# Kernel optimization log

Measured on AMD Instinct MI355X. Metric: run time of the kernel, lower is better.

Reference implementation:

```python
import jax, jax.numpy as jnp
import numpy as np

P, K, L = 2048, 10, 3        # pairs, paths-per-pair (cap 10), max path length
E, H = 256, 512              # kg_embed_dim, node_dim
N_ENT, N_REL = 10000, 200
N_HEADS = 4


def setup_inputs() -> dict:
    key = jax.random.key(0)
    ks = jax.random.split(key, 20)
    s = 0.05  # weight scale for numerical stability
    return {
        'rel_idx': jax.random.randint(ks[0], (P, K, L), 0, N_REL, dtype=jnp.int32),
        'ent_idx': jax.random.randint(ks[1], (P, K, L), 0, N_ENT, dtype=jnp.int32),
        'path_lens': jax.random.randint(ks[2], (P, K), 0, L + 1, dtype=jnp.int32),
        'rel_table': jax.random.normal(ks[3], (N_REL, E), jnp.float32),
        'ent_table': jax.random.normal(ks[4], (N_ENT, E), jnp.float32),
        'kg_proj_w': jax.random.normal(ks[5], (H, E), jnp.float32) * s,
        'kg_proj_b': jax.random.normal(ks[6], (H,), jnp.float32) * s,
        'w_ih': jax.random.normal(ks[7], (4 * H, 2 * H), jnp.float32) * s,
        'w_hh': jax.random.normal(ks[8], (4 * H, H), jnp.float32) * s,
        'b_ih': jax.random.normal(ks[9], (4 * H,), jnp.float32) * s,
        'b_hh': jax.random.normal(ks[10], (4 * H,), jnp.float32) * s,
        'attn_in_w': jax.random.normal(ks[11], (3 * H, H), jnp.float32) * s,
        'attn_in_b': jax.random.normal(ks[12], (3 * H,), jnp.float32) * s,
        'attn_out_w': jax.random.normal(ks[13], (H, H), jnp.float32) * s,
        'attn_out_b': jax.random.normal(ks[14], (H,), jnp.float32) * s,
        'path_proj_w': jax.random.normal(ks[15], (H, H), jnp.float32) * s,
        'path_proj_b': jax.random.normal(ks[16], (H,), jnp.float32) * s,
    }


def _forward(rel_idx, ent_idx, path_lens, rel_table, ent_table, kg_proj_w, kg_proj_b,
             w_ih, w_hh, b_ih, b_hh, attn_in_w, attn_in_b, attn_out_w, attn_out_b,
             path_proj_w, path_proj_b):
    # --- encode_path, batched over all P*K paths ---
    rel_e = rel_table[rel_idx]                      # [P,K,L,E]
    ent_e = ent_table[ent_idx]                      # [P,K,L,E]
    rel_p = rel_e @ kg_proj_w.T + kg_proj_b         # [P,K,L,H]
    ent_p = ent_e @ kg_proj_w.T + kg_proj_b
    x = jnp.concatenate([rel_p, ent_p], axis=-1)    # [P,K,L,2H]
    Npk = P * K
    xs = x.reshape(Npk, L, 2 * H).transpose(1, 0, 2)  # [L,N,2H]

    h0 = jnp.zeros((Npk, H), x.dtype)
    c0 = jnp.zeros((Npk, H), x.dtype)

    def lstm_step(carry, x_t):
        h, c = carry
        g = x_t @ w_ih.T + b_ih + h @ w_hh.T + b_hh   # [N,4H], torch gate order i,f,g,o
        i, f, gg, o = jnp.split(g, 4, axis=-1)
        c = jax.nn.sigmoid(f) * c + jax.nn.sigmoid(i) * jnp.tanh(gg)
        h = jax.nn.sigmoid(o) * jnp.tanh(c)
        return (h, c), h

    _, hs = jax.lax.scan(lstm_step, (h0, c0), xs)     # [L,N,H]
    hs = hs.transpose(1, 0, 2)                        # [N,L,H]
    lens = path_lens.reshape(Npk)                     # [N]
    last = jnp.clip(lens - 1, 0, L - 1)
    h_last = jnp.take_along_axis(hs, last[:, None, None], axis=1)[:, 0]  # [N,H]
    path_emb = jnp.where(lens[:, None] > 0, h_last, 0.0).reshape(P, K, H)

    # --- per-pair multi-head self-attention over K path embeddings ---
    wq, wk, wv = jnp.split(attn_in_w, 3, axis=0)
    bq, bk, bv = jnp.split(attn_in_b, 3, axis=0)
    Dh = H // N_HEADS
    q = (path_emb @ wq.T + bq).reshape(P, K, N_HEADS, Dh)
    k = (path_emb @ wk.T + bk).reshape(P, K, N_HEADS, Dh)
    v = (path_emb @ wv.T + bv).reshape(P, K, N_HEADS, Dh)
    scores = jnp.einsum('pqhd,pkhd->phqk', q, k) / jnp.sqrt(jnp.array(Dh, x.dtype))
    attn = jax.nn.softmax(scores, axis=-1)
    ctx = jnp.einsum('phqk,pkhd->pqhd', attn, v).reshape(P, K, H)
    attn_out = ctx @ attn_out_w.T + attn_out_b        # [P,K,H]
    agg = attn_out.mean(axis=1)                       # [P,H]  (aggregated.mean(dim=1))
    return agg @ path_proj_w.T + path_proj_b          # [P,H]


def reference(rel_idx, ent_idx, path_lens, rel_table, ent_table, kg_proj_w, kg_proj_b,
              w_ih, w_hh, b_ih, b_hh, attn_in_w, attn_in_b, attn_out_w, attn_out_b,
              path_proj_w, path_proj_b):
    return _forward(rel_idx, ent_idx, path_lens, rel_table, ent_table, kg_proj_w,
                    kg_proj_b, w_ih, w_hh, b_ih, b_hh, attn_in_w, attn_in_b,
                    attn_out_w, attn_out_b, path_proj_w, path_proj_b)
```

## Files before the change

### kernel.cpp

```cpp
#include <hip/hip_runtime.h>
#include <cstdint>
#include <cstddef>

#define PP 2048
#define KK 10
#define HH 512
#define NPK (PP*KK)
#define ENT_PAD 10112
#define REL_PAD 256
#define HALF_PAIRS 1024
#define HALF_ROWS (HALF_PAIRS*KK)

using f32x4  = __attribute__((ext_vector_type(4))) float;
using short8 = __attribute__((ext_vector_type(8))) short;

__device__ __forceinline__ float fexp2(float x) {
#if __has_builtin(__builtin_amdgcn_exp2f)
    return __builtin_amdgcn_exp2f(x);
#else
    return __exp2f(x);
#endif
}
__device__ __forceinline__ float frcp(float x) {
#if __has_builtin(__builtin_amdgcn_rcpf)
    return __builtin_amdgcn_rcpf(x);
#else
    return 1.0f / x;
#endif
}
#define LOG2E  1.4426950408889634f
#define LOG2E2 2.8853900817779268f
__device__ __forceinline__ float sigf(float x) {
    return frcp(1.0f + fexp2(-LOG2E * x));
}
__device__ __forceinline__ float tanhf_f(float x) {
    float xc = fminf(fmaxf(x, -9.0f), 9.0f);
    float e = fexp2(LOG2E2 * xc);
    return (e - 1.0f) * frcp(e + 1.0f);
}

__device__ __forceinline__ ushort f2bf(float x) {
    union { float f; uint32_t u; } v; v.f = x;
    uint32_t r = v.u + 0x7FFF + ((v.u >> 16) & 1);
    return (ushort)(r >> 16);
}
__device__ __forceinline__ float bf2f(ushort u) {
    union { uint32_t u; float f; } v; v.u = ((uint32_t)u) << 16;
    return v.f;
}

__global__ __launch_bounds__(256) void perm_bias2(int* __restrict__ perm_p,
                                                  int* __restrict__ perm_q,
                                                  float* __restrict__ bihh_q,
                                                  const float* __restrict__ b_ih,
                                                  const float* __restrict__ b_hh) {
    int i = blockIdx.x * 256 + threadIdx.x;
    if (i < 2048) {
        int uh = i >> 6, g = (i >> 4) & 3, ul = i & 15;
        perm_p[i] = g * 512 + uh * 16 + ul;
        int u = i >> 2, gq = i & 3;
        int oldq = gq * 512 + u;
        perm_q[i] = oldq;
        bihh_q[i] = b_ih[oldq] + b_hh[oldq];
    }
}

__global__ __launch_bounds__(256) void transpose_k(const float* __restrict__ src,
                                                   float* __restrict__ dst, int R, int C) {
    __shared__ float t[32][33];
    int bx = blockIdx.x * 32, by = blockIdx.y * 32;
    int x = threadIdx.x & 31, y = threadIdx.x >> 5;
    for (int i = y; i < 32; i += 8) {
        int r = by + i, c = bx + x;
        if (r < R && c < C) t[i][x] = src[(size_t)r * C + c];
    }
    __syncthreads();
    for (int i = y; i < 32; i += 8) {
        int c = bx + i, r = by + x;
        if (r < R && c < C) dst[(size_t)c * R + r] = t[x][i];
    }
}

__global__ __launch_bounds__(256) void rowdot(const float* __restrict__ A, int lda,
                                              const float* __restrict__ vec, int Kd,
                                              const float* __restrict__ add1,
                                              float* __restrict__ out, int M) {
    int w = threadIdx.x >> 6, lane = threadIdx.x & 63;
    int row = blockIdx.x * 4 + w;
    if (row >= M) return;
    float acc = 0.f;
    for (int k = lane; k < Kd; k += 64) acc += A[(size_t)row * lda + k] * vec[k];
    for (int off = 32; off; off >>= 1) acc += __shfl_down(acc, off, 64);
    if (lane == 0) {
        float r = acc;
        if (add1) r += add1[row];
        out[row] = r;
    }
}

__global__ __launch_bounds__(256) void f2bf_split2d(const float* __restrict__ src,
                                                    int lda, int col0,
                                                    ushort* __restrict__ hi,
                                                    ushort* __restrict__ lo,
                                                    int nsrc_rows, int ncols, int ndst_rows,
                                                    const int* __restrict__ perm) {
    int i = blockIdx.x * 256 + threadIdx.x;
    int nc4 = ncols >> 2;
    if (i >= ndst_rows * nc4) return;
    int row = i / nc4, c4 = i % nc4;
    ushort4 h = make_ushort4(0, 0, 0, 0), l = make_ushort4(0, 0, 0, 0);
    if (row < nsrc_rows) {
        int sr = perm ? perm[row] : row;
        float4 v = *reinterpret_cast<const float4*>(src + (size_t)sr * lda + col0 + c4 * 4);
        h = make_ushort4(f2bf(v.x), f2bf(v.y), f2bf(v.z), f2bf(v.w));
        l = make_ushort4(f2bf(v.x - bf2f(h.x)), f2bf(v.y - bf2f(h.y)),
                         f2bf(v.z - bf2f(h.z)), f2bf(v.w - bf2f(h.w)));
    }
    reinterpret_cast<ushort4*>(hi)[i] = h;
    reinterpret_cast<ushort4*>(lo)[i] = l;
}

__global__ __launch_bounds__(256) void f2bf_k(const float* __restrict__ s,
                                              ushort* __restrict__ d, int n4) {
    int i = blockIdx.x * 256 + threadIdx.x;
    if (i < n4) {
        float4 v = reinterpret_cast<const float4*>(s)[i];
        reinterpret_cast<ushort4*>(d)[i] = make_ushort4(f2bf(v.x), f2bf(v.y), f2bf(v.z), f2bf(v.w));
    }
}

__global__ __launch_bounds__(256) void f2bf_perm_rows(const float* __restrict__ s,
                                                      ushort* __restrict__ d,
                                                      const int* __restrict__ perm,
                                                      int nrows, int ncols4) {
    int i = blockIdx.x * 256 + threadIdx.x;
    if (i >= nrows * ncols4) return;
    int row = i / ncols4, c4 = i % ncols4;
    int sr = perm[row];
    float4 v = reinterpret_cast<const float4*>(s + (size_t)sr * ncols4 * 4)[c4];
    reinterpret_cast<ushort4*>(d + (size_t)row * ncols4 * 4)[c4] =
        make_ushort4(f2bf(v.x), f2bf(v.y), f2bf(v.z), f2bf(v.w));
}

__global__ __launch_bounds__(256) void gemm_bf16(
    const ushort* __restrict__ A, const ushort* __restrict__ B,
    float* __restrict__ C, int M, int N, int K, int ldc,
    const float* __restrict__ bias)
{
    __shared__ ushort As[128 * 64];
    __shared__ ushort Bs[128 * 64];
    int tid = threadIdx.x;
    int lane = tid & 63;
    int w = tid >> 6;
    int wr = w >> 1, wc = w & 1;
    int col0 = blockIdx.x * 128, row0 = blockIdx.y * 128;

    f32x4 acc[4][4];
#pragma unroll
    for (int m = 0; m < 4; ++m)
#pragma unroll
        for (int n = 0; n < 4; ++n) acc[m][n] = {0.f, 0.f, 0.f, 0.f};

    int rA = lane & 15;
    int kq = lane >> 4;

    for (int kt = 0; kt < K; kt += 64) {
#pragma unroll
        for (int it = 0; it < 4; ++it) {
            int c = it * 256 + tid;
            int row = c >> 3, ch = c & 7;
            int cs = ch ^ (row & 7);
            uint4 va = *reinterpret_cast<const uint4*>(A + (size_t)(row0 + row) * K + kt + ch * 8);
            *reinterpret_cast<uint4*>(&As[(size_t)row * 64 + cs * 8]) = va;
            uint4 vb = *reinterpret_cast<const uint4*>(B + (size_t)(col0 + row) * K + kt + ch * 8);
            *reinterpret_cast<uint4*>(&Bs[(size_t)row * 64 + cs * 8]) = vb;
        }
        __syncthreads();
#pragma unroll
        for (int s = 0; s < 2; ++s) {
            int csw = (s * 4 + kq) ^ (rA & 7);
            short8 af[4], bfr[4];
#pragma unroll
            for (int m = 0; m < 4; ++m) {
                int rowA = wr * 64 + m * 16 + rA;
                af[m] = *reinterpret_cast<const short8*>(&As[(size_t)rowA * 64 + csw * 8]);
            }
#pragma unroll
            for (int n = 0; n < 4; ++n) {
                int rowB = wc * 64 + n * 16 + rA;
                bfr[n] = *reinterpret_cast<const short8*>(&Bs[(size_t)rowB * 64 + csw * 8]);
            }
#pragma unroll
            for (int m = 0; m < 4; ++m)
#pragma unroll
                for (int n = 0; n < 4; ++n)
                    acc[m][n] = __builtin_amdgcn_mfma_f32_16x16x32_bf16(af[m], bfr[n], acc[m][n], 0, 0, 0);
        }
        __syncthreads();
    }
#pragma unroll
    for (int n = 0; n < 4; ++n) {
        int gcol = col0 + wc * 64 + n * 16 + rA;
        float bv = bias ? bias[gcol] : 0.f;
#pragma unroll
        for (int m = 0; m < 4; ++m) {
            int grow0 = row0 + wr * 64 + m * 16 + kq * 4;
#pragma unroll
            for (int r = 0; r < 4; ++r)
                C[(size_t)(grow0 + r) * ldc + gcol] = acc[m][n][r] + bv;
        }
    }
}

__global__ __launch_bounds__(256) void gemm_bf16s(
    const ushort* __restrict__ Ah, const ushort* __restrict__ Al,
    const ushort* __restrict__ Bh, const ushort* __restrict__ Bl,
    float* __restrict__ C, ushort* __restrict__ Chi, ushort* __restrict__ Clo,
    int M, int N, int K, int ldc,
    const float* __restrict__ bias)
{
    __shared__ ushort Ash[128 * 64];
    __shared__ ushort Asl[128 * 64];
    __shared__ ushort Bsh[128 * 64];
    __shared__ ushort Bsl[128 * 64];
    int tid = threadIdx.x;
    int lane = tid & 63;
    int w = tid >> 6;
    int wr = w >> 1, wc = w & 1;
    int col0 = blockIdx.x * 128, row0 = blockIdx.y * 128;

    f32x4 acc[4][4];
#pragma unroll
    for (int m = 0; m < 4; ++m)
#pragma unroll
        for (int n = 0; n < 4; ++n) acc[m][n] = {0.f, 0.f, 0.f, 0.f};

    int rA = lane & 15;
    int kq = lane >> 4;

    for (int kt = 0; kt < K; kt += 64) {
#pragma unroll
        for (int it = 0; it < 4; ++it) {
            int c = it * 256 + tid;
            int row = c >> 3, ch = c & 7;
            int cs = ch ^ (row & 7);
            size_t ga = (size_t)(row0 + row) * K + kt + ch * 8;
            size_t gb = (size_t)(col0 + row) * K + kt + ch * 8;
            size_t la = (size_t)row * 64 + cs * 8;
            *reinterpret_cast<uint4*>(&Ash[la]) = *reinterpret_cast<const uint4*>(Ah + ga);
            *reinterpret_cast<uint4*>(&Asl[la]) = *reinterpret_cast<const uint4*>(Al + ga);
            *reinterpret_cast<uint4*>(&Bsh[la]) = *reinterpret_cast<const uint4*>(Bh + gb);
            *reinterpret_cast<uint4*>(&Bsl[la]) = *reinterpret_cast<const uint4*>(Bl + gb);
        }
        __syncthreads();
#pragma unroll
        for (int s = 0; s < 2; ++s) {
            int csw = (s * 4 + kq) ^ (rA & 7);
            short8 xh[4], yh[4], t4[4];
#pragma unroll
            for (int m = 0; m < 4; ++m) {
                int rowA = wr * 64 + m * 16 + rA;
                xh[m] = *reinterpret_cast<const short8*>(&Ash[(size_t)rowA * 64 + csw * 8]);
            }
#pragma unroll
            for (int n = 0; n < 4; ++n) {
                int rowB = wc * 64 + n * 16 + rA;
                yh[n] = *reinterpret_cast<const short8*>(&Bsh[(size_t)rowB * 64 + csw * 8]);
            }
#pragma unroll
            for (int m = 0; m < 4; ++m)
#pragma unroll
                for (int n = 0; n < 4; ++n)
                    acc[m][n] = __builtin_amdgcn_mfma_f32_16x16x32_bf16(xh[m], yh[n], acc[m][n], 0, 0, 0);
#pragma unroll
            for (int n = 0; n < 4; ++n) {
                int rowB = wc * 64 + n * 16 + rA;
                t4[n] = *reinterpret_cast<const short8*>(&Bsl[(size_t)rowB * 64 + csw * 8]);
            }
#pragma unroll
            for (int m = 0; m < 4; ++m)
#pragma unroll
                for (int n = 0; n < 4; ++n)
                    acc[m][n] = __builtin_amdgcn_mfma_f32_16x16x32_bf16(xh[m], t4[n], acc[m][n], 0, 0, 0);
#pragma unroll
            for (int m = 0; m < 4; ++m) {
                int rowA = wr * 64 + m * 16 + rA;
                t4[m] = *reinterpret_cast<const short8*>(&Asl[(size_t)rowA * 64 + csw * 8]);
            }
#pragma unroll
            for (int m = 0; m < 4; ++m)
#pragma unroll
                for (int n = 0; n < 4; ++n)
                    acc[m][n] = __builtin_amdgcn_mfma_f32_16x16x32_bf16(t4[m], yh[n], acc[m][n], 0, 0, 0);
        }
        __syncthreads();
    }
#pragma unroll
    for (int n = 0; n < 4; ++n) {
        int gcol = col0 + wc * 64 + n * 16 + rA;
        float bv = bias ? bias[gcol] : 0.f;
#pragma unroll
        for (int m = 0; m < 4; ++m) {
            int grow0 = row0 + wr * 64 + m * 16 + kq * 4;
#pragma unroll
            for (int r = 0; r < 4; ++r) {
                float v = acc[m][n][r] + bv;
                size_t idx = (size_t)(grow0 + r) * ldc + gcol;
                if (C) C[idx] = v;
                if (Chi) {
                    ushort h = f2bf(v);
                    Chi[idx] = h;
                    Clo[idx] = f2bf(v - bf2f(h));
                }
            }
        }
    }
}

__global__ __launch_bounds__(256) void gemm_lstm(
    const ushort* __restrict__ A, const ushort* __restrict__ B,
    const float* __restrict__ relg, const float* __restrict__ entg,
    const int* __restrict__ rel_idx, const int* __restrict__ ent_idx,
    const int* __restrict__ lens_,
    ushort* __restrict__ hbuf, float* __restrict__ cbuf, ushort* __restrict__ pemb,
    int t)
{
    __shared__ ushort As[128 * 64];
    __shared__ ushort Bs[128 * 64];
    const int K = 512;
    int L = blockIdx.x;
    int swz = (L & 7) * 320 + (L >> 3);
    int bx = swz & 15, by = swz >> 4;
    int tid = threadIdx.x;
    int lane = tid & 63;
    int w = tid >> 6;
    int wr = w >> 1, wc = w & 1;
    int col0 = bx * 128, row0 = by * 128;

    f32x4 acc[4][4];
#pragma unroll
    for (int m = 0; m < 4; ++m)
#pragma unroll
        for (int n = 0; n < 4; ++n) acc[m][n] = {0.f, 0.f, 0.f, 0.f};

    int rA = lane & 15;
    int kq = lane >> 4;

    for (int kt = 0; kt < K; kt += 64) {
#pragma unroll
        for (int it = 0; it < 4; ++it) {
            int c = it * 256 + tid;
            int row = c >> 3, ch = c & 7;
            int cs = ch ^ (row & 7);
            uint4 va = *reinterpret_cast<const uint4*>(A + (size_t)(row0 + row) * K + kt + ch * 8);
            *reinterpret_cast<uint4*>(&As[(size_t)row * 64 + cs * 8]) = va;
            uint4 vb = *reinterpret_cast<const uint4*>(B + (size_t)(col0 + row) * K + kt + ch * 8);
            *reinterpret_cast<uint4*>(&Bs[(size_t)row * 64 + cs * 8]) = vb;
        }
        __syncthreads();
#pragma unroll
        for (int s = 0; s < 2; ++s) {
            int csw = (s * 4 + kq) ^ (rA & 7);
            short8 af[4], bfr[4];
#pragma unroll
            for (int m = 0; m < 4; ++m) {
                int rowA = wr * 64 + m * 16 + rA;
                af[m] = *reinterpret_cast<const short8*>(&As[(size_t)rowA * 64 + csw * 8]);
            }
#pragma unroll
            for (int n = 0; n < 4; ++n) {
                int rowB = wc * 64 + n * 16 + rA;
                bfr[n] = *reinterpret_cast<const short8*>(&Bs[(size_t)rowB * 64 + csw * 8]);
            }
#pragma unroll
            for (int m = 0; m < 4; ++m)
#pragma unroll
                for (int n = 0; n < 4; ++n)
                    acc[m][n] = __builtin_amdgcn_mfma_f32_16x16x32_bf16(af[m], bfr[n], acc[m][n], 0, 0, 0);
        }
        __syncthreads();
    }

    int uh = bx * 2 + wc;
    int u  = uh * 16 + rA;
    const float4* rel4 = reinterpret_cast<const float4*>(relg);
    const float4* ent4 = reinterpret_cast<const float4*>(entg);
#pragma unroll
    for (int m = 0; m < 4; ++m) {
#pragma unroll
        for (int r = 0; r < 4; ++r) {
            int n = row0 + wr * 64 + m * 16 + kq * 4 + r;
            int ri = rel_idx[n * 3 + t];
            int ei = ent_idx[n * 3 + t];
            float4 rv = rel4[(size_t)ri * 512 + u];
            float4 ev = ent4[(size_t)ei * 512 + u];
            float gi = acc[m][0][r] + rv.x + ev.x;
            float gf = acc[m][1][r] + rv.y + ev.y;
            float gg = acc[m][2][r] + rv.z + ev.z;
            float go = acc[m][3][r] + rv.w + ev.w;
            float cold = cbuf[(size_t)n * 512 + u];
            float cn = sigf(gf) * cold + sigf(gi) * tanhf_f(gg);
            float hn = sigf(go) * tanhf_f(cn);
            cbuf[(size_t)n * 512 + u] = cn;
            ushort hu = f2bf(hn);
            hbuf[(size_t)n * 512 + u] = hu;
            int len = lens_[n];
            int last = len - 1;
            if (last < 0) last = 0;
            if (last > 2) last = 2;
            if (last == t) pemb[(size_t)n * 512 + u] = (len > 0) ? hu : (ushort)0;
        }
    }
}

__global__ __launch_bounds__(256) void lstm_t0(
    const float* __restrict__ relg, const float* __restrict__ entg,
    const int* __restrict__ rel_idx, const int* __restrict__ ent_idx,
    const int* __restrict__ lens_,
    ushort* __restrict__ hbuf, float* __restrict__ cbuf, ushort* __restrict__ pemb,
    int nrows)
{
    int gid = blockIdx.x * 256 + threadIdx.x;
    if (gid >= nrows * 128) return;
    int nl = gid >> 7, q = gid & 127;
    int ri = rel_idx[nl * 3];
    int ei = ent_idx[nl * 3];
    const float4* rg = reinterpret_cast<const float4*>(relg) + (size_t)ri * 512;
    const float4* eg = reinterpret_cast<const float4*>(entg) + (size_t)ei * 512;
    float4 cn, hn;
#pragma unroll
    for (int j = 0; j < 4; ++j) {
        float4 a = rg[q * 4 + j];
        float4 b = eg[q * 4 + j];
        float gi = a.x + b.x, gg = a.z + b.z, go = a.w + b.w;
        float c = sigf(gi) * tanhf_f(gg);
        float h = sigf(go) * tanhf_f(c);
        (&cn.x)[j] = c;
        (&hn.x)[j] = h;
    }
    reinterpret_cast<float4*>(cbuf + (size_t)nl * 512)[q] = cn;
    ushort4 hu = make_ushort4(f2bf(hn.x), f2bf(hn.y), f2bf(hn.z), f2bf(hn.w));
    reinterpret_cast<ushort4*>(hbuf + (size_t)nl * 512)[q] = hu;
    int len = lens_[nl];
    int last = len - 1;
    if (last < 0) last = 0;
    if (last > 2) last = 2;
    if (last == 0) {
        ushort4 pv = (len > 0) ? hu : make_ushort4(0, 0, 0, 0);
        reinterpret_cast<ushort4*>(pemb + (size_t)nl * 512)[q] = pv;
    }
}

__global__ __launch_bounds__(256) void attn_kernel(const float* __restrict__ qkv,
                                                   ushort* __restrict__ mch,
                                                   ushort* __restrict__ mcl, int pair0)
{
    __shared__ float qk[10][1024];
    __shared__ float sc[4][10][10];
    __shared__ float wb[4][10];
    int tid = threadIdx.x;
    const float* base = qkv + (size_t)blockIdx.x * 10 * 1536;
    for (int i = tid; i < 2560; i += 256) {
        int row = i >> 8, c4 = i & 255;
        reinterpret_cast<float4*>(&qk[row][0])[c4] =
            reinterpret_cast<const float4*>(base + (size_t)row * 1536)[c4];
    }
    __syncthreads();
    const float scale = 0.08838834764831845f;
    for (int idx = tid; idx < 400; idx += 256) {
        int h = idx / 100, rem = idx % 100, qi = rem / 10, ki = rem % 10;
        const float* qp = &qk[qi][h * 128];
        const float* kp = &qk[ki][512 + h * 128];
        float a = 0.f;
        for (int d = 0; d < 128; ++d) a += qp[d] * kp[d];
        sc[h][qi][ki] = a * scale;
    }
    __syncthreads();
    if (tid < 40) {
        int h = tid / 10, qi = tid % 10;
        float m = -1e30f;
        for (int ki = 0; ki < 10; ++ki) m = fmaxf(m, sc[h][qi][ki]);
        float ex[10]; float s = 0.f;
        for (int ki = 0; ki < 10; ++ki) { ex[ki] = fexp2(LOG2E * (sc[h][qi][ki] - m)); s += ex[ki]; }
        float inv = frcp(s);
        for (int ki = 0; ki < 10; ++ki) sc[h][qi][ki] = ex[ki] * inv;
    }
    __syncthreads();
    if (tid < 40) {
        int h = tid / 10, ki = tid % 10;
        float s = 0.f;
        for (int qi = 0; qi < 10; ++qi) s += sc[h][qi][ki];
        wb[h][ki] = s * 0.1f;
    }
    __syncthreads();
    for (int e = tid; e < 512; e += 256) {
        int h = e >> 7, d = e & 127;
        float a = 0.f;
        for (int ki = 0; ki < 10; ++ki)
            a += wb[h][ki] * base[(size_t)ki * 1536 + 1024 + h * 128 + d];
        size_t idx = (size_t)(pair0 + blockIdx.x) * 512 + e;
        ushort hh = f2bf(a);
        mch[idx] = hh;
        mcl[idx] = f2bf(a - bf2f(hh));
    }
}

extern "C" void kernel_launch(void* const* d_in, const int* in_sizes, int n_in,
                              void* d_out, int out_size, void* d_ws, size_t ws_size,
                              hipStream_t stream)
{
    const int* rel_idx     = (const int*)d_in[0];
    const int* ent_idx     = (const int*)d_in[1];
    const int* path_lens   = (const int*)d_in[2];
    const float* rel_table = (const float*)d_in[3];
    const float* ent_table = (const float*)d_in[4];
    const float* kg_proj_w = (const float*)d_in[5];
    const float* kg_proj_b = (const float*)d_in[6];
    const float* w_ih      = (const float*)d_in[7];
    const float* w_hh      = (const float*)d_in[8];
    const float* b_ih      = (const float*)d_in[9];
    const float* b_hh      = (const float*)d_in[10];
    const float* attn_in_w = (const float*)d_in[11];
    const float* attn_in_b = (const float*)d_in[12];
    const float* attn_out_w = (const float*)d_in[13];
    const float* attn_out_b = (const float*)d_in[14];
    const float* path_proj_w = (const float*)d_in[15];
    const float* path_proj_b = (const float*)d_in[16];
    float* out = (float*)d_out;
    (void)in_sizes; (void)n_in; (void)out_size; (void)ws_size;

    float* ws = (float*)d_ws;
    size_t off = 0;
    auto alloc = [&](size_t n) { float* p = ws + off; off += (n + 63) & ~(size_t)63; return p; };
    int*    perm_p = (int*)alloc(2048);
    int*    perm_q = (int*)alloc(2048);
    float*  bihh   = alloc(2048);
    float*  bcomb  = alloc(512);
    float*  relg   = alloc((size_t)REL_PAD * 2048);
    float*  entg   = alloc((size_t)ENT_PAD * 2048);
    ushort* whhB   = (ushort*)alloc((size_t)2048 * 256);
    ushort* aiwB   = (ushort*)alloc((size_t)1536 * 256);
    ushort* pch    = (ushort*)alloc((size_t)NPK * 256);
    ushort* Wch    = (ushort*)alloc((size_t)512 * 256);
    ushort* Wcl    = (ushort*)alloc((size_t)512 * 256);
    ushort* mch    = (ushort*)alloc((size_t)PP * 256);
    ushort* mcl    = (ushort*)alloc((size_t)PP * 256);
    float* R = alloc((size_t)21000000);

    size_t ro = 0;
    auto ral = [&](size_t n) { float* p = R + ro; ro += n; return p; };
    ushort* kgWh  = (ushort*)ral(65536);   ushort* kgWl  = (ushort*)ral(65536);
    ushort* relBh = (ushort*)ral(32768);   ushort* relBl = (ushort*)ral(32768);
    ushort* entBh = (ushort*)ral(1294336); ushort* entBl = (ushort*)ral(1294336);
    ushort* wrelh = (ushort*)ral(524288);  ushort* wrell = (ushort*)ral(524288);
    ushort* wenth = (ushort*)ral(524288);  ushort* wentl = (ushort*)ral(524288);
    ushort* rel_ph = (ushort*)ral(65536);   ushort* rel_pl = (ushort*)ral(65536);
    ushort* ent_ph = (ushort*)ral(2588672); ushort* ent_pl = (ushort*)ral(2588672);
    float*  aoT    = ral(262144);
    ushort* pph  = (ushort*)ral(131072); ushort* ppl  = (ushort*)ral(131072);
    ushort* aoTh = (ushort*)ral(131072); ushort* aoTl = (ushort*)ral(131072);
    float*  cb = R;
    ushort* hA = (ushort*)(R + 10485760);
    ushort* hB = (ushort*)(R + 15728640);
    float*  qkv = R;

    auto split = [&](const float* src, int lda, int col0, ushort* hi, ushort* lo,
                     int nsrc, int ncols, int ndst, const int* pm) {
        int total = ndst * (ncols / 4);
        f2bf_split2d<<<(total + 255) / 256, 256, 0, stream>>>(src, lda, col0, hi, lo, nsrc, ncols, ndst, pm);
    };
    auto gemms = [&](const ushort* Ah, const ushort* Al, const ushort* Bh, const ushort* Bl,
                     float* Cp, ushort* Chi, ushort* Clo,
                     int M, int N, int Kd, int ldc, const float* bias) {
        gemm_bf16s<<<dim3((unsigned)(N / 128), (unsigned)(M / 128)), 256, 0, stream>>>(
            Ah, Al, Bh, Bl, Cp, Chi, Clo, M, N, Kd, ldc, bias);
    };

    perm_bias2<<<8, 256, 0, stream>>>(perm_p, perm_q, bihh, b_ih, b_hh);
    transpose_k<<<dim3(16, 16), 256, 0, stream>>>(attn_out_w, aoT, 512, 512);
    split(kg_proj_w, 256, 0, kgWh, kgWl, 512, 256, 512, nullptr);
    split(rel_table, 256, 0, relBh, relBl, 200, 256, REL_PAD, nullptr);
    split(ent_table, 256, 0, entBh, entBl, 10000, 256, ENT_PAD, nullptr);
    split(w_ih, 1024, 0,   wrelh, wrell, 2048, 512, 2048, perm_q);
    split(w_ih, 1024, 512, wenth, wentl, 2048, 512, 2048, perm_q);
    split(path_proj_w, 512, 0, pph, ppl, 512, 512, 512, nullptr);
    split(aoT, 512, 0, aoTh, aoTl, 512, 512, 512, nullptr);
    f2bf_perm_rows<<<1024, 256, 0, stream>>>(w_hh, whhB, perm_p, 2048, 128);
    f2bf_k<<<768, 256, 0, stream>>>(attn_in_w, aiwB, 1536 * 128);
    rowdot<<<128, 256, 0, stream>>>(path_proj_w, 512, attn_out_b, 512, path_proj_b, bcomb, 512);

    gemms(relBh, relBl, kgWh, kgWl, nullptr, rel_ph, rel_pl, REL_PAD, 512, 256, 512, kg_proj_b);
    gemms(entBh, entBl, kgWh, kgWl, nullptr, ent_ph, ent_pl, ENT_PAD, 512, 256, 512, kg_proj_b);
    gemms(rel_ph, rel_pl, wrelh, wrell, relg, nullptr, nullptr, REL_PAD, 2048, 512, 2048, bihh);
    gemms(ent_ph, ent_pl, wenth, wentl, entg, nullptr, nullptr, ENT_PAD, 2048, 512, 2048, nullptr);
    gemms(pph, ppl, aoTh, aoTl, nullptr, Wch, Wcl, 512, 512, 512, 512, nullptr);

    lstm_t0<<<(NPK * 128) / 256, 256, 0, stream>>>(
        relg, entg, rel_idx, ent_idx, path_lens, hA, cb, pch, NPK);
    gemm_lstm<<<2560, 256, 0, stream>>>(
        hA, whhB, relg, entg, rel_idx, ent_idx, path_lens, hB, cb, pch, 1);
    gemm_lstm<<<2560, 256, 0, stream>>>(
        hB, whhB, relg, entg, rel_idx, ent_idx, path_lens, hA, cb, pch, 2);

    for (int h = 0; h < 2; ++h) {
        gemm_bf16<<<dim3(12, 80), 256, 0, stream>>>(
            pch + (size_t)h * HALF_ROWS * 512, aiwB, qkv, HALF_ROWS, 1536, 512, 1536, attn_in_b);
        attn_kernel<<<HALF_PAIRS, 256, 0, stream>>>(qkv, mch, mcl, h * HALF_PAIRS);
    }

    gemms(mch, mcl, Wch, Wcl, out, nullptr, nullptr, 2048, 512, 512, 512, bcomb);
}
```

Baseline: 678.3 us.

## Compact LSTM rows by path length to skip finished paths in later steps

```diff
diff --git a/kernel.cpp b/kernel.cpp
--- a/kernel.cpp
+++ b/kernel.cpp
@@ -47,6 +47,36 @@
 __device__ __forceinline__ float bf2f(ushort u) {
     union { uint32_t u; float f; } v; v.u = ((uint32_t)u) << 16;
     return v.f;
+}
+
+__global__ __launch_bounds__(256) void class_hist(const int* __restrict__ lens,
+                                                  int* __restrict__ meta, int n) {
+    int i = blockIdx.x * 256 + threadIdx.x;
+    if (i < n) {
+        int len = lens[i];
+        int b = (len == 3) ? 0 : ((len == 2) ? 1 : 2);
+        atomicAdd(&meta[b], 1);
+    }
+}
+__global__ void class_ofs(int* __restrict__ meta) {
+    if (threadIdx.x == 0 && blockIdx.x == 0) {
+        int n3 = meta[0], n2 = meta[1];
+        meta[8] = 0; meta[9] = n3; meta[10] = n3 + n2;
+        meta[6] = n3 + n2; meta[7] = n3;
+    }
+}
+__global__ __launch_bounds__(256) void class_scatter(const int* __restrict__ lens,
+                                                     int* __restrict__ meta,
+                                                     int* __restrict__ rowmap,
+                                                     int* __restrict__ inv, int n) {
+    int i = blockIdx.x * 256 + threadIdx.x;
+    if (i < n) {
+        int len = lens[i];
+        int b = (len == 3) ? 0 : ((len == 2) ? 1 : 2);
+        int pos = meta[8 + b] + atomicAdd(&meta[3 + b], 1);
+        rowmap[pos] = i;
+        inv[i] = pos;
+    }
 }
 
 __global__ __launch_bounds__(256) void perm_bias2(int* __restrict__ perm_p,
@@ -322,20 +352,25 @@
     const float* __restrict__ relg, const float* __restrict__ entg,
     const int* __restrict__ rel_idx, const int* __restrict__ ent_idx,
     const int* __restrict__ lens_,
+    const int* __restrict__ rowmap, const int* __restrict__ meta,
     ushort* __restrict__ hbuf, float* __restrict__ cbuf, ushort* __restrict__ pemb,
     int t)
 {
     __shared__ ushort As[128 * 64];
     __shared__ ushort Bs[128 * 64];
     const int K = 512;
+    int act    = (t == 1) ? meta[6] : meta[7];
+    int wr_lim = (t == 1) ? meta[7] : 0;
     int L = blockIdx.x;
     int swz = (L & 7) * 320 + (L >> 3);
     int bx = swz & 15, by = swz >> 4;
+    int row0 = by * 128;
+    if (row0 >= act) return;
+    int col0 = bx * 128;
     int tid = threadIdx.x;
     int lane = tid & 63;
     int w = tid >> 6;
     int wr = w >> 1, wc = w & 1;
-    int col0 = bx * 128, row0 = by * 128;
 
     f32x4 acc[4][4];
 #pragma unroll
@@ -389,26 +424,30 @@
     for (int m = 0; m < 4; ++m) {
 #pragma unroll
         for (int r = 0; r < 4; ++r) {
-            int n = row0 + wr * 64 + m * 16 + kq * 4 + r;
-            int ri = rel_idx[n * 3 + t];
-            int ei = ent_idx[n * 3 + t];
+            int nc = row0 + wr * 64 + m * 16 + kq * 4 + r;
+            if (nc >= act) continue;
+            int orig = rowmap[nc];
+            int ri = rel_idx[orig * 3 + t];
+            int ei = ent_idx[orig * 3 + t];
             float4 rv = rel4[(size_t)ri * 512 + u];
             float4 ev = ent4[(size_t)ei * 512 + u];
             float gi = acc[m][0][r] + rv.x + ev.x;
             float gf = acc[m][1][r] + rv.y + ev.y;
             float gg = acc[m][2][r] + rv.z + ev.z;
             float go = acc[m][3][r] + rv.w + ev.w;
-            float cold = cbuf[(size_t)n * 512 + u];
+            float cold = cbuf[(size_t)nc * 512 + u];
             float cn = sigf(gf) * cold + sigf(gi) * tanhf_f(gg);
             float hn = sigf(go) * tanhf_f(cn);
-            cbuf[(size_t)n * 512 + u] = cn;
             ushort hu = f2bf(hn);
-            hbuf[(size_t)n * 512 + u] = hu;
-            int len = lens_[n];
+            if (nc < wr_lim) {
+                cbuf[(size_t)nc * 512 + u] = cn;
+                hbuf[(size_t)nc * 512 + u] = hu;
+            }
+            int len = lens_[orig];
             int last = len - 1;
             if (last < 0) last = 0;
             if (last > 2) last = 2;
-            if (last == t) pemb[(size_t)n * 512 + u] = (len > 0) ? hu : (ushort)0;
+            if (last == t) pemb[(size_t)orig * 512 + u] = (len > 0) ? hu : (ushort)0;
         }
     }
 }
@@ -417,6 +456,7 @@
     const float* __restrict__ relg, const float* __restrict__ entg,
     const int* __restrict__ rel_idx, const int* __restrict__ ent_idx,
     const int* __restrict__ lens_,
+    const int* __restrict__ inv, const int* __restrict__ meta,
     ushort* __restrict__ hbuf, float* __restrict__ cbuf, ushort* __restrict__ pemb,
     int nrows)
 {
@@ -438,15 +478,19 @@
         (&cn.x)[j] = c;
         (&hn.x)[j] = h;
     }
-    reinterpret_cast<float4*>(cbuf + (size_t)nl * 512)[q] = cn;
-    ushort4 hu = make_ushort4(f2bf(hn.x), f2bf(hn.y), f2bf(hn.z), f2bf(hn.w));
-    reinterpret_cast<ushort4*>(hbuf + (size_t)nl * 512)[q] = hu;
+    int pos = inv[nl];
+    if (pos < meta[6]) {
+        reinterpret_cast<float4*>(cbuf + (size_t)pos * 512)[q] = cn;
+        ushort4 hq = make_ushort4(f2bf(hn.x), f2bf(hn.y), f2bf(hn.z), f2bf(hn.w));
+        reinterpret_cast<ushort4*>(hbuf + (size_t)pos * 512)[q] = hq;
+    }
     int len = lens_[nl];
     int last = len - 1;
     if (last < 0) last = 0;
     if (last > 2) last = 2;
     if (last == 0) {
-        ushort4 pv = (len > 0) ? hu : make_ushort4(0, 0, 0, 0);
+        ushort4 pv = make_ushort4(0, 0, 0, 0);
+        if (len > 0) pv = make_ushort4(f2bf(hn.x), f2bf(hn.y), f2bf(hn.z), f2bf(hn.w));
         reinterpret_cast<ushort4*>(pemb + (size_t)nl * 512)[q] = pv;
     }
 }
@@ -532,6 +576,9 @@
     float* ws = (float*)d_ws;
     size_t off = 0;
     auto alloc = [&](size_t n) { float* p = ws + off; off += (n + 63) & ~(size_t)63; return p; };
+    int*    meta   = (int*)alloc(64);
+    int*    rowmap = (int*)alloc(NPK);
+    int*    invm   = (int*)alloc(NPK);
     int*    perm_p = (int*)alloc(2048);
     int*    perm_q = (int*)alloc(2048);
     float*  bihh   = alloc(2048);
@@ -576,6 +623,11 @@
             Ah, Al, Bh, Bl, Cp, Chi, Clo, M, N, Kd, ldc, bias);
     };
 
+    hipMemsetAsync(meta, 0, 64, stream);
+    class_hist<<<(NPK + 255) / 256, 256, 0, stream>>>(path_lens, meta, NPK);
+    class_ofs<<<1, 64, 0, stream>>>(meta);
+    class_scatter<<<(NPK + 255) / 256, 256, 0, stream>>>(path_lens, meta, rowmap, invm, NPK);
+
     perm_bias2<<<8, 256, 0, stream>>>(perm_p, perm_q, bihh, b_ih, b_hh);
     transpose_k<<<dim3(16, 16), 256, 0, stream>>>(attn_out_w, aoT, 512, 512);
     split(kg_proj_w, 256, 0, kgWh, kgWl, 512, 256, 512, nullptr);
@@ -596,11 +648,11 @@
     gemms(pph, ppl, aoTh, aoTl, nullptr, Wch, Wcl, 512, 512, 512, 512, nullptr);
 
     lstm_t0<<<(NPK * 128) / 256, 256, 0, stream>>>(
-        relg, entg, rel_idx, ent_idx, path_lens, hA, cb, pch, NPK);
+        relg, entg, rel_idx, ent_idx, path_lens, invm, meta, hA, cb, pch, NPK);
     gemm_lstm<<<2560, 256, 0, stream>>>(
-        hA, whhB, relg, entg, rel_idx, ent_idx, path_lens, hB, cb, pch, 1);
+        hA, whhB, relg, entg, rel_idx, ent_idx, path_lens, rowmap, meta, hB, cb, pch, 1);
     gemm_lstm<<<2560, 256, 0, stream>>>(
-        hB, whhB, relg, entg, rel_idx, ent_idx, path_lens, hA, cb, pch, 2);
+        hB, whhB, relg, entg, rel_idx, ent_idx, path_lens, rowmap, meta, hA, cb, pch, 2);
 
     for (int h = 0; h < 2; ++h) {
         gemm_bf16<<<dim3(12, 80), 256, 0, stream>>>(
```

Result: slower. 1.055 ms (+55.5%).
